# Performance work log

Measured on AMD Instinct MI355X. Metric: run time of the kernel, lower is better.

Reference implementation:

```python
import math
import jax, jax.numpy as jnp
import numpy as np

B, S, D = 1, 2048, 4096
HQ, HKV = 32, 8
HD = D // HQ          # 128
N_REP = HQ // HKV     # 4
ROPE_BASE = 10000.0


def setup_inputs() -> dict:
    key = jax.random.key(0)
    ks = jax.random.split(key, 6)
    x = jax.random.normal(ks[0], (B, S, D), dtype=jnp.float32)
    scale = 0.02
    wq = jax.random.normal(ks[1], (D, HQ * HD), dtype=jnp.float32) * scale
    wk = jax.random.normal(ks[2], (D, HKV * HD), dtype=jnp.float32) * scale
    wv = jax.random.normal(ks[3], (D, HKV * HD), dtype=jnp.float32) * scale
    wo = jax.random.normal(ks[4], (HQ * HD, D), dtype=jnp.float32) * scale
    # rotary freqs: freqs_cis = exp(i * t * theta_j), theta_j = base^{-2j/hd}
    inv_freq = 1.0 / (ROPE_BASE ** (jnp.arange(0, HD, 2, dtype=jnp.float32) / HD))
    t = jnp.arange(S, dtype=jnp.float32)
    ang = t[:, None] * inv_freq[None, :]          # [S, HD/2]
    cos = jnp.cos(ang)
    sin = jnp.sin(ang)
    # additive causal mask [S, S]: 0 on/below diagonal, -1e9 above
    mask = jnp.triu(jnp.full((S, S), -1e9, dtype=jnp.float32), k=1)
    return {"x": x, "wq": wq, "wk": wk, "wv": wv, "wo": wo,
            "cos": cos, "sin": sin, "mask": mask}


def _rope(t, cos, sin):
    # t: [B, S, H, HD]; complex mult on (even, odd) pairs
    te, to = t[..., 0::2], t[..., 1::2]
    c = cos[None, :, None, :]
    s = sin[None, :, None, :]
    oe = te * c - to * s
    oo = te * s + to * c
    return jnp.stack([oe, oo], axis=-1).reshape(t.shape)


def reference(x, wq, wk, wv, wo, cos, sin, mask):
    b, s, _ = x.shape
    xq = (x @ wq).reshape(b, s, HQ, HD)
    xk = (x @ wk).reshape(b, s, HKV, HD)
    xv = (x @ wv).reshape(b, s, HKV, HD)
    xq = _rope(xq, cos, sin)
    xk = _rope(xk, cos, sin)
    # repeat_kv == repeat_interleave along head dim
    xk = jnp.repeat(xk, N_REP, axis=2)
    xv = jnp.repeat(xv, N_REP, axis=2)
    # [B, H, S, HD]
    xq = xq.transpose(0, 2, 1, 3)
    xk = xk.transpose(0, 2, 1, 3)
    xv = xv.transpose(0, 2, 1, 3)
    scores = jnp.einsum('bhqd,bhkd->bhqk', xq, xk) / math.sqrt(HD)
    scores = scores + mask[None, None, :, :]
    probs = jax.nn.softmax(scores.astype(jnp.float32), axis=-1).astype(xq.dtype)
    out = jnp.einsum('bhqk,bhkd->bhqd', probs, xv)
    out = out.transpose(0, 2, 1, 3).reshape(b, s, HQ * HD)
    return out @ wo
```

## Files before the change

### kernel.cpp

```cpp
#include <hip/hip_runtime.h>
#include <hip/hip_bf16.h>
#include <stdint.h>

#define S_LEN 2048
#define DMODEL 4096
#define N_HQ 32
#define N_HKV 8
#define HD 128
#define NQKV 6144
#define KOFF 4096
#define VOFF 5120

typedef __bf16 bf16x8 __attribute__((ext_vector_type(8)));
typedef __bf16 bf16x4 __attribute__((ext_vector_type(4)));
typedef float f32x4 __attribute__((ext_vector_type(4)));

static __device__ __forceinline__ f32x4 mfma16(bf16x8 a, bf16x8 b, f32x4 c) {
  return __builtin_amdgcn_mfma_f32_16x16x32_bf16(a, b, c, 0, 0, 0);
}

typedef const __attribute__((address_space(1))) void* gas_cvp;
typedef __attribute__((address_space(3))) void* las_vp;

__global__ __launch_bounds__(256) void cvt_f32_bf16(
    const float* __restrict__ in, __bf16* __restrict__ out)
{
  int i = blockIdx.x * 256 + threadIdx.x;
  float4 v = ((const float4*)in)[i];
  bf16x4 o = { (__bf16)v.x, (__bf16)v.y, (__bf16)v.z, (__bf16)v.w };
  *(bf16x4*)(out + 4*(size_t)i) = o;
}

__global__ __launch_bounds__(256) void transpose_cvt_k(
    const float* __restrict__ in, __bf16* __restrict__ out,
    int in_stride, int out_stride, float scale)
{
  __shared__ float tile[32][33];
  int tx = threadIdx.x & 31;
  int ty = threadIdx.x >> 5;
  size_t r0 = (size_t)blockIdx.y * 32;
  size_t c0 = (size_t)blockIdx.x * 32;
#pragma unroll
  for (int i = 0; i < 4; i++)
    tile[ty + i*8][tx] = in[(r0 + ty + i*8) * in_stride + c0 + tx];
  __syncthreads();
#pragma unroll
  for (int i = 0; i < 4; i++)
    out[(c0 + ty + i*8) * out_stride + r0 + tx] = (__bf16)(tile[tx][ty + i*8] * scale);
}

__global__ __launch_bounds__(256) void transpose_k(
    const uint16_t* __restrict__ in, uint16_t* __restrict__ out,
    int in_stride, int out_stride)
{
  __shared__ uint16_t tile[32][33];
  int tx = threadIdx.x & 31;
  int ty = threadIdx.x >> 5;
  size_t r0 = (size_t)blockIdx.y * 32;
  size_t c0 = (size_t)blockIdx.x * 32;
#pragma unroll
  for (int i = 0; i < 4; i++)
    tile[ty + i*8][tx] = in[(r0 + ty + i*8) * in_stride + c0 + tx];
  __syncthreads();
#pragma unroll
  for (int i = 0; i < 4; i++)
    out[(c0 + ty + i*8) * out_stride + r0 + tx] = tile[tx][ty + i*8];
}

#define BKG 64
template <typename OutT>
__global__ __launch_bounds__(256, 3) void gemm_bt(
    const __bf16* __restrict__ A,
    const __bf16* __restrict__ Bt,
    OutT* __restrict__ C,
    int M, int N, int K)
{
  __shared__ __attribute__((aligned(16))) __bf16 Asl[128*BKG];
  __shared__ __attribute__((aligned(16))) __bf16 Bsl[128*BKG];
  int tid = threadIdx.x;
  int lane = tid & 63, wave = tid >> 6;
  int wm = wave >> 1, wn = wave & 1;
  int row16 = lane & 15, quad = lane >> 4;
  size_t m0 = (size_t)blockIdx.y * 128;
  size_t n0 = (size_t)blockIdx.x * 128;
  f32x4 acc[4][4] = {};

  for (int k0 = 0; k0 < K; k0 += BKG) {
    __syncthreads();
#pragma unroll
    for (int c = 0; c < 4; c++) {
      int u = c*256 + tid;
      int r = u >> 3;
      int swz = (u & 7) ^ (r & 7);
      const __bf16* ga = A + (m0 + r) * (size_t)K + k0 + swz*8;
      char* la = (char*)Asl + (size_t)(c*256 + wave*64) * 16;
      __builtin_amdgcn_global_load_lds((gas_cvp)ga, (las_vp)la, 16, 0, 0);
      const __bf16* gb = Bt + (n0 + r) * (size_t)K + k0 + swz*8;
      char* lb = (char*)Bsl + (size_t)(c*256 + wave*64) * 16;
      __builtin_amdgcn_global_load_lds((gas_cvp)gb, (las_vp)lb, 16, 0, 0);
    }
    __syncthreads();

#pragma unroll
    for (int kk = 0; kk < 2; kk++) {
      int sw = ((kk*4 + quad) ^ (row16 & 7)) * 8;
      bf16x8 af[4], bfr[4];
#pragma unroll
      for (int i = 0; i < 4; i++)
        af[i] = *(const bf16x8*)&Asl[(wm*64 + i*16 + row16)*BKG + sw];
#pragma unroll
      for (int j = 0; j < 4; j++)
        bfr[j] = *(const bf16x8*)&Bsl[(wn*64 + j*16 + row16)*BKG + sw];
#pragma unroll
      for (int i = 0; i < 4; i++)
#pragma unroll
        for (int j = 0; j < 4; j++)
          acc[i][j] = mfma16(af[i], bfr[j], acc[i][j]);
    }
  }

#pragma unroll
  for (int i = 0; i < 4; i++)
#pragma unroll
    for (int j = 0; j < 4; j++)
#pragma unroll
      for (int r = 0; r < 4; r++) {
        size_t row = m0 + wm*64 + i*16 + quad*4 + r;
        size_t col = n0 + wn*64 + j*16 + row16;
        C[row * (size_t)N + col] = (OutT)acc[i][j][r];
      }
}

__global__ __launch_bounds__(256) void rope_k(
    __bf16* __restrict__ qkv,
    const float* __restrict__ cosb,
    const float* __restrict__ sinb)
{
  int idx = blockIdx.x * 256 + threadIdx.x;
  const int NQP = S_LEN * N_HQ * 64;
  __bf16* p;
  int s, i;
  if (idx < NQP) {
    s = idx >> 11;
    int rem = idx & 2047;
    int h = rem >> 6;
    i = rem & 63;
    p = qkv + (size_t)s * NQKV + h*HD + 2*i;
  } else {
    int j = idx - NQP;
    s = j >> 9;
    int rem = j & 511;
    int h = rem >> 6;
    i = rem & 63;
    p = qkv + (size_t)s * NQKV + KOFF + h*HD + 2*i;
  }
  float te = (float)p[0], to = (float)p[1];
  float c = cosb[s*64 + i], sn = sinb[s*64 + i];
  p[0] = (__bf16)(te*c - to*sn);
  p[1] = (__bf16)(te*sn + to*c);
}

#define KB 64
#define PSTR 72
__global__ __launch_bounds__(256, 2) void attn_k(
    const __bf16* __restrict__ qkv,
    const __bf16* __restrict__ vt,
    __bf16* __restrict__ attnout)
{
  __shared__ __attribute__((aligned(16))) __bf16 Kl[KB*HD];
  __shared__ __attribute__((aligned(16))) __bf16 Vl[HD*KB];
  __shared__ __attribute__((aligned(16))) __bf16 Pl[4*32*PSTR];
  int tid = threadIdx.x;
  int lane = tid & 63, wave = tid >> 6;
  int row16 = lane & 15, quad = lane >> 4;

  int b = blockIdx.x;
  int h = b & 31;
  int j = b >> 5;
  int pr = j >> 1, hb = j & 1;
  int qt_h = 15 - pr;
  int qt_l = pr;
  int hkv = h >> 2;
  int h0 = qt_h*128 + hb*64 + wave*16;
  int l0 = qt_l*128 + hb*64 + wave*16;
  int ktd_h = 2*qt_h + hb;
  int ktd_l = 2*qt_l + hb;
  int nkt = ktd_h + 1;

  bf16x8 qf[2][4];
#pragma unroll
  for (int c = 0; c < 4; c++) {
    qf[0][c] = *(const bf16x8*)&qkv[(size_t)(h0 + row16)*NQKV + h*HD + c*32 + quad*8];
    qf[1][c] = *(const bf16x8*)&qkv[(size_t)(l0 + row16)*NQKV + h*HD + c*32 + quad*8];
  }

  f32x4 acc[2][8] = {};
  float lsum[2][4] = {};

  __bf16* Pw = &Pl[wave*32*PSTR];
  for (int kt = 0; kt < nkt; kt++) {
    int kb = kt*KB;
    __syncthreads();
#pragma unroll
    for (int c = 0; c < 4; c++) {
      int u = c*256 + tid;
      int kr = u >> 4;
      int kp = (u & 15) ^ (kr & 15);
      const __bf16* gk = &qkv[(size_t)(kb+kr)*NQKV + KOFF + hkv*HD + kp*8];
      char* lk = (char*)Kl + (size_t)(c*256 + wave*64) * 16;
      __builtin_amdgcn_global_load_lds((gas_cvp)gk, (las_vp)lk, 16, 0, 0);
      int dd = u >> 3;
      int vp = (u & 7) ^ (dd & 7);
      const __bf16* gv = &vt[(size_t)(hkv*HD + dd)*S_LEN + kb + vp*8];
      char* lv = (char*)Vl + (size_t)(c*256 + wave*64) * 16;
      __builtin_amdgcn_global_load_lds((gas_cvp)gv, (las_vp)lv, 16, 0, 0);
    }
    __syncthreads();

    int lightOn = (kt <= ktd_l);

    f32x4 s[2][4] = {};
#pragma unroll
    for (int c = 0; c < 4; c++) {
      bf16x8 kf[4];
#pragma unroll
      for (int jt = 0; jt < 4; jt++) {
        int pc = (c*4 + quad) ^ row16;
        kf[jt] = *(const bf16x8*)&Kl[(jt*16 + row16)*HD + pc*8];
      }
#pragma unroll
      for (int jt = 0; jt < 4; jt++)
        s[0][jt] = mfma16(qf[0][c], kf[jt], s[0][jt]);
      if (lightOn)
#pragma unroll
        for (int jt = 0; jt < 4; jt++)
          s[1][jt] = mfma16(qf[1][c], kf[jt], s[1][jt]);
    }

    if (kt == ktd_h) {
#pragma unroll
      for (int r = 0; r < 4; r++) {
        int rowl = quad*4 + r;
        int row_g = h0 + rowl;
#pragma unroll
        for (int jt = 0; jt < 4; jt++) {
          int col_g = kb + jt*16 + row16;
          float e = (col_g <= row_g) ? exp2f(s[0][jt][r]) : 0.0f;
          lsum[0][r] += e;
          Pw[rowl*PSTR + jt*16 + row16] = (__bf16)e;
        }
      }
    } else {
#pragma unroll
      for (int r = 0; r < 4; r++) {
        int rowl = quad*4 + r;
#pragma unroll
        for (int jt = 0; jt < 4; jt++) {
          float e = exp2f(s[0][jt][r]);
          lsum[0][r] += e;
          Pw[rowl*PSTR + jt*16 + row16] = (__bf16)e;
        }
      }
    }
    if (lightOn) {
      if (kt == ktd_l) {
#pragma unroll
        for (int r = 0; r < 4; r++) {
          int rowl = quad*4 + r;
          int row_g = l0 + rowl;
#pragma unroll
          for (int jt = 0; jt < 4; jt++) {
            int col_g = kb + jt*16 + row16;
            float e = (col_g <= row_g) ? exp2f(s[1][jt][r]) : 0.0f;
            lsum[1][r] += e;
            Pw[(16+rowl)*PSTR + jt*16 + row16] = (__bf16)e;
          }
        }
      } else {
#pragma unroll
        for (int r = 0; r < 4; r++) {
          int rowl = quad*4 + r;
#pragma unroll
          for (int jt = 0; jt < 4; jt++) {
            float e = exp2f(s[1][jt][r]);
            lsum[1][r] += e;
            Pw[(16+rowl)*PSTR + jt*16 + row16] = (__bf16)e;
          }
        }
      }
    }

#pragma unroll
    for (int kk = 0; kk < 2; kk++) {
      bf16x8 pa0 = *(const bf16x8*)&Pw[(row16)*PSTR + kk*32 + quad*8];
      bf16x8 pa1 = *(const bf16x8*)&Pw[(16+row16)*PSTR + kk*32 + quad*8];
#pragma unroll
      for (int ct = 0; ct < 8; ct++) {
        int pv = (kk*4 + quad) ^ (row16 & 7);
        bf16x8 vb = *(const bf16x8*)&Vl[(ct*16 + row16)*KB + pv*8];
        acc[0][ct] = mfma16(pa0, vb, acc[0][ct]);
        if (lightOn) acc[1][ct] = mfma16(pa1, vb, acc[1][ct]);
      }
    }
  }

#pragma unroll
  for (int mt = 0; mt < 2; mt++)
#pragma unroll
    for (int r = 0; r < 4; r++) {
      float l = lsum[mt][r];
      l += __shfl_xor(l, 1);
      l += __shfl_xor(l, 2);
      l += __shfl_xor(l, 4);
      l += __shfl_xor(l, 8);
      lsum[mt][r] = 1.0f / l;
    }
#pragma unroll
  for (int mt = 0; mt < 2; mt++) {
    int base = (mt == 0) ? h0 : l0;
#pragma unroll
    for (int r = 0; r < 4; r++) {
      size_t qrow = (size_t)base + quad*4 + r;
      float inv = lsum[mt][r];
#pragma unroll
      for (int ct = 0; ct < 8; ct++)
        attnout[qrow*DMODEL + h*HD + ct*16 + row16] = (__bf16)(acc[mt][ct][r] * inv);
    }
  }
}

extern "C" void kernel_launch(void* const* d_in, const int* in_sizes, int n_in,
                              void* d_out, int out_size, void* d_ws, size_t ws_size,
                              hipStream_t stream) {
  const float* x    = (const float*)d_in[0];
  const float* wq   = (const float*)d_in[1];
  const float* wk   = (const float*)d_in[2];
  const float* wv   = (const float*)d_in[3];
  const float* wo   = (const float*)d_in[4];
  const float* cosb = (const float*)d_in[5];
  const float* sinb = (const float*)d_in[6];
  float* out = (float*)d_out;

  __bf16* ws   = (__bf16*)d_ws;
  __bf16* Wt   = ws;
  __bf16* Wot  = ws;
  __bf16* xb   = Wt  + (size_t)NQKV*DMODEL;
  __bf16* attn = xb;
  __bf16* qkv  = xb  + (size_t)S_LEN*DMODEL;
  __bf16* vt   = qkv + (size_t)S_LEN*NQKV;

  const float QSCALE = 0.12751295866442674f;

  cvt_f32_bf16<<<8192,256,0,stream>>>(x, xb);
  transpose_cvt_k<<<dim3(128,128),256,0,stream>>>(wq, Wt, 4096, 4096, QSCALE);
  transpose_cvt_k<<<dim3(32,128),256,0,stream>>>(wk, Wt + (size_t)4096*4096, 1024, 4096, 1.0f);
  transpose_cvt_k<<<dim3(32,128),256,0,stream>>>(wv, Wt + (size_t)5120*4096, 1024, 4096, 1.0f);

  gemm_bt<__bf16><<<dim3(NQKV/128, S_LEN/128),256,0,stream>>>(xb, Wt, qkv, S_LEN, NQKV, DMODEL);

  rope_k<<<20480,256,0,stream>>>(qkv, cosb, sinb);

  transpose_k<<<dim3(32,64),256,0,stream>>>((const uint16_t*)(qkv + VOFF), (uint16_t*)vt, NQKV, S_LEN);

  transpose_cvt_k<<<dim3(128,128),256,0,stream>>>(wo, Wot, 4096, 4096, 1.0f);

  attn_k<<<512,256,0,stream>>>(qkv, vt, attn);

  gemm_bt<float><<<dim3(DMODEL/128, S_LEN/128),256,0,stream>>>(attn, Wot, out, S_LEN, DMODEL, DMODEL);
}
```

Measured before the change: 480.2 us.

## Fuse RoPE into QKV GEMM epilogue and merge weight transpose kernels

```diff
diff --git a/kernel.cpp b/kernel.cpp
--- a/kernel.cpp
+++ b/kernel.cpp
@@ -31,22 +31,51 @@
   *(bf16x4*)(out + 4*(size_t)i) = o;
 }
 
-__global__ __launch_bounds__(256) void transpose_cvt_k(
-    const float* __restrict__ in, __bf16* __restrict__ out,
-    int in_stride, int out_stride, float scale)
-{
-  __shared__ float tile[32][33];
-  int tx = threadIdx.x & 31;
-  int ty = threadIdx.x >> 5;
-  size_t r0 = (size_t)blockIdx.y * 32;
-  size_t c0 = (size_t)blockIdx.x * 32;
-#pragma unroll
-  for (int i = 0; i < 4; i++)
-    tile[ty + i*8][tx] = in[(r0 + ty + i*8) * in_stride + c0 + tx];
+static __device__ __forceinline__ void tr_tile(
+    const float* __restrict__ src, __bf16* __restrict__ dst,
+    int ins, int outs, float scale, int r0, int c0,
+    uint32_t (*pt)[37], int t)
+{
+  int c = t & 31, r2 = t >> 5;
+#pragma unroll
+  for (int i = 0; i < 4; i++) {
+    int rp = r2 + 8*i;
+    const float* s0 = src + (size_t)(r0 + 2*rp) * ins + c0 + c;
+    float f0 = s0[0];
+    float f1 = s0[ins];
+    uint16_t lo = __builtin_bit_cast(uint16_t, (__bf16)(f0 * scale));
+    uint16_t hi = __builtin_bit_cast(uint16_t, (__bf16)(f1 * scale));
+    pt[c][rp] = (uint32_t)lo | ((uint32_t)hi << 16);
+  }
   __syncthreads();
-#pragma unroll
-  for (int i = 0; i < 4; i++)
-    out[(c0 + ty + i*8) * out_stride + r0 + tx] = (__bf16)(tile[tx][ty + i*8] * scale);
+  int oc = t >> 3, og = t & 7;
+#pragma unroll
+  for (int i = 0; i < 4; i++) {
+    int rp = og + 8*i;
+    *(uint32_t*)&dst[(size_t)(c0 + oc) * outs + r0 + 2*rp] = pt[oc][rp];
+  }
+}
+
+__global__ __launch_bounds__(256) void prep_w_qkv(
+    const float* __restrict__ wq, const float* __restrict__ wk,
+    const float* __restrict__ wv, __bf16* __restrict__ Wt)
+{
+  __shared__ uint32_t pt[32][37];
+  int bx = blockIdx.x;
+  const float* src; int ins; float scale; int obase;
+  if (bx < 128)      { src = wq; ins = 4096; scale = 0.12751295866442674f; obase = 0; }
+  else if (bx < 160) { src = wk; ins = 1024; scale = 1.0f; obase = 4096; bx -= 128; }
+  else               { src = wv; ins = 1024; scale = 1.0f; obase = 5120; bx -= 160; }
+  tr_tile(src, Wt + (size_t)obase * 4096, ins, 4096, scale,
+          (int)blockIdx.y * 64, bx * 32, pt, threadIdx.x);
+}
+
+__global__ __launch_bounds__(256) void prep_wo(
+    const float* __restrict__ wo, __bf16* __restrict__ Wot)
+{
+  __shared__ uint32_t pt[32][37];
+  tr_tile(wo, Wot, 4096, 4096, 1.0f,
+          (int)blockIdx.y * 64, (int)blockIdx.x * 32, pt, threadIdx.x);
 }
 
 __global__ __launch_bounds__(256) void transpose_k(
@@ -68,12 +97,13 @@
 }
 
 #define BKG 64
-template <typename OutT>
+template <typename OutT, bool ROPE>
 __global__ __launch_bounds__(256, 3) void gemm_bt(
     const __bf16* __restrict__ A,
     const __bf16* __restrict__ Bt,
     OutT* __restrict__ C,
-    int M, int N, int K)
+    int M, int N, int K,
+    const float* __restrict__ cosb, const float* __restrict__ sinb)
 {
   __shared__ __attribute__((aligned(16))) __bf16 Asl[128*BKG];
   __shared__ __attribute__((aligned(16))) __bf16 Bsl[128*BKG];
@@ -119,6 +149,7 @@
     }
   }
 
+  const bool doRope = ROPE && (n0 < 5120);
 #pragma unroll
   for (int i = 0; i < 4; i++)
 #pragma unroll
@@ -127,37 +158,16 @@
       for (int r = 0; r < 4; r++) {
         size_t row = m0 + wm*64 + i*16 + quad*4 + r;
         size_t col = n0 + wn*64 + j*16 + row16;
-        C[row * (size_t)N + col] = (OutT)acc[i][j][r];
-      }
-}
-
-__global__ __launch_bounds__(256) void rope_k(
-    __bf16* __restrict__ qkv,
-    const float* __restrict__ cosb,
-    const float* __restrict__ sinb)
-{
-  int idx = blockIdx.x * 256 + threadIdx.x;
-  const int NQP = S_LEN * N_HQ * 64;
-  __bf16* p;
-  int s, i;
-  if (idx < NQP) {
-    s = idx >> 11;
-    int rem = idx & 2047;
-    int h = rem >> 6;
-    i = rem & 63;
-    p = qkv + (size_t)s * NQKV + h*HD + 2*i;
-  } else {
-    int j = idx - NQP;
-    s = j >> 9;
-    int rem = j & 511;
-    int h = rem >> 6;
-    i = rem & 63;
-    p = qkv + (size_t)s * NQKV + KOFF + h*HD + 2*i;
-  }
-  float te = (float)p[0], to = (float)p[1];
-  float c = cosb[s*64 + i], sn = sinb[s*64 + i];
-  p[0] = (__bf16)(te*c - to*sn);
-  p[1] = (__bf16)(te*sn + to*c);
+        float v = acc[i][j][r];
+        if (doRope) {
+          float other = __shfl_xor(v, 1);
+          int ii = (int)(col & 127) >> 1;
+          float cc = cosb[row*64 + ii];
+          float ss = sinb[row*64 + ii];
+          v = (lane & 1) ? (other*ss + v*cc) : (v*cc - other*ss);
+        }
+        C[row * (size_t)N + col] = (OutT)v;
+      }
 }
 
 #define KB 64
@@ -267,11 +277,10 @@
 #pragma unroll
         for (int r = 0; r < 4; r++) {
           int rowl = quad*4 + r;
-          int row_g = l0 + rowl;
 #pragma unroll
           for (int jt = 0; jt < 4; jt++) {
             int col_g = kb + jt*16 + row16;
-            float e = (col_g <= row_g) ? exp2f(s[1][jt][r]) : 0.0f;
+            float e = (col_g <= l0 + rowl) ? exp2f(s[1][jt][r]) : 0.0f;
             lsum[1][r] += e;
             Pw[(16+rowl)*PSTR + jt*16 + row16] = (__bf16)e;
           }
@@ -349,22 +358,18 @@
   __bf16* qkv  = xb  + (size_t)S_LEN*DMODEL;
   __bf16* vt   = qkv + (size_t)S_LEN*NQKV;
 
-  const float QSCALE = 0.12751295866442674f;
-
   cvt_f32_bf16<<<8192,256,0,stream>>>(x, xb);
-  transpose_cvt_k<<<dim3(128,128),256,0,stream>>>(wq, Wt, 4096, 4096, QSCALE);
-  transpose_cvt_k<<<dim3(32,128),256,0,stream>>>(wk, Wt + (size_t)4096*4096, 1024, 4096, 1.0f);
-  transpose_cvt_k<<<dim3(32,128),256,0,stream>>>(wv, Wt + (size_t)5120*4096, 1024, 4096, 1.0f);
-
-  gemm_bt<__bf16><<<dim3(NQKV/128, S_LEN/128),256,0,stream>>>(xb, Wt, qkv, S_LEN, NQKV, DMODEL);
-
-  rope_k<<<20480,256,0,stream>>>(qkv, cosb, sinb);
+  prep_w_qkv<<<dim3(192,64),256,0,stream>>>(wq, wk, wv, Wt);
+
+  gemm_bt<__bf16, true><<<dim3(NQKV/128, S_LEN/128),256,0,stream>>>(
+      xb, Wt, qkv, S_LEN, NQKV, DMODEL, cosb, sinb);
 
   transpose_k<<<dim3(32,64),256,0,stream>>>((const uint16_t*)(qkv + VOFF), (uint16_t*)vt, NQKV, S_LEN);
 
-  transpose_cvt_k<<<dim3(128,128),256,0,stream>>>(wo, Wot, 4096, 4096, 1.0f);
+  prep_wo<<<dim3(128,64),256,0,stream>>>(wo, Wot);
 
   attn_k<<<512,256,0,stream>>>(qkv, vt, attn);
 
-  gemm_bt<float><<<dim3(DMODEL/128, S_LEN/128),256,0,stream>>>(attn, Wot, out, S_LEN, DMODEL, DMODEL);
-}
+  gemm_bt<float, false><<<dim3(DMODEL/128, S_LEN/128),256,0,stream>>>(
+      attn, Wot, out, S_LEN, DMODEL, DMODEL, nullptr, nullptr);
+}
```

Result: no change. 480.8 us (+0.1%).
